# Performance work log

Measured on AMD Instinct MI355X. Metric: run time of the kernel, lower is better.

## Reference

```python
import jax, jax.numpy as jnp
import numpy as np

B, N, D, P = 4, 512, 512, 128

def setup_inputs() -> dict:
    key = jax.random.key(0)
    ks = jax.random.split(key, 8)
    s = lambda fan_in: 1.0 / np.sqrt(fan_in)
    inp = {
        "input": jax.random.normal(ks[0], (B, N, D), dtype=jnp.float32),
        # bigram projections (weights stored [in, out]; torch Linear is [out, in])
        "Wl": jax.random.uniform(ks[1], (D, P), jnp.float32, -s(D), s(D)),
        "bl": jnp.zeros((P,), jnp.float32),  # zeroed in initialize_parameters
        "Wr": jax.random.uniform(ks[2], (D, P), jnp.float32, -s(D), s(D)),  # no bias
        "Wo": jax.random.uniform(ks[3], (P, 1), jnp.float32, -s(P), s(P)),
        "bo": jnp.zeros((1,), jnp.float32),
        # start builder MLP
        "Ws1": jax.random.uniform(ks[4], (D, P), jnp.float32, -s(D), s(D)),
        "bs1": jnp.zeros((P,), jnp.float32),
        "Ws2": jax.random.uniform(ks[5], (P, 1), jnp.float32, -s(P), s(P)),
        "bs2": jnp.zeros((1,), jnp.float32),
        # end builder MLP
        "We1": jax.random.uniform(ks[6], (D, P), jnp.float32, -s(D), s(D)),
        "be1": jnp.zeros((P,), jnp.float32),
        "We2": jax.random.uniform(ks[7], (P, 1), jnp.float32, -s(P), s(P)),
        "be2": jnp.zeros((1,), jnp.float32),
    }
    return inp


def reference(input, Wl, bl, Wr, Wo, bo, Ws1, bs1, Ws2, bs2, We1, be1, We2, be2):
    # start / end unigram scores: [B, N, 1]
    start = jnp.maximum(input @ Ws1 + bs1, 0.0) @ Ws2 + bs2
    end = jnp.maximum(input @ We1 + be1, 0.0) @ We2 + be2
    # bigram scores
    left = input @ Wl + bl   # [B, N, P]
    right = input @ Wr       # [B, N, P]
    # left.unsqueeze(1) + right.unsqueeze(2) -> [B, N, N, P]
    proj = left[:, None, :, :] + right[:, :, None, :]
    bigram = jnp.maximum(proj, 0.0) @ Wo + bo  # [B, N, N, 1]
    return (bigram, start, end)
```

## Files before the change

kernel.cpp:

```cpp
#include <hip/hip_runtime.h>

typedef unsigned short ushort_t;
using f32x4  = __attribute__((ext_vector_type(4))) float;
using bf16x8 = __attribute__((ext_vector_type(8))) short;
using u16x8  = __attribute__((ext_vector_type(8))) unsigned short;

constexpr int Bc = 4;
constexpr int Nc = 512;
constexpr int Dc = 512;
constexpr int Pc = 128;
constexpr int ROWS = Bc * Nc;

__device__ inline unsigned short f2bf(float f) {
    unsigned u = __builtin_bit_cast(unsigned, f);
    unsigned r = u + 0x7fffu + ((u >> 16) & 1u);
    return (unsigned short)(r >> 16);
}

__device__ inline void gload_lds16(const void* g, void* l) {
    __builtin_amdgcn_global_load_lds(
        (const __attribute__((address_space(1))) unsigned int*)g,
        (__attribute__((address_space(3))) unsigned int*)l, 16, 0, 0);
}

__global__ __launch_bounds__(256) void convert_kernel(
    const float* __restrict__ input,
    const float* __restrict__ Wl,  const float* __restrict__ Wr,
    const float* __restrict__ Ws1, const float* __restrict__ We1,
    ushort_t* __restrict__ inBF2, ushort_t* __restrict__ WcatT2)
{
    const int bx = blockIdx.x, t = threadIdx.x;
    __shared__ float T[64][68];

    if (bx < 256) {
        const int mt = bx >> 3, ks = bx & 7;
        const int c = t & 7, r0 = t >> 3;
        const float* src = input + (size_t)(mt * 64) * Dc + ks * 64;
        ushort_t* dstc = inBF2 + ((size_t)(mt * 8 + ks) * 8 + c) * 512;
        #pragma unroll
        for (int h = 0; h < 2; ++h) {
            const int r = r0 + h * 32;
            const float* s = src + (size_t)r * Dc + c * 8;
            float4 v0 = *(const float4*)s;
            float4 v1 = *(const float4*)(s + 4);
            u16x8 o;
            o[0] = f2bf(v0.x); o[1] = f2bf(v0.y); o[2] = f2bf(v0.z); o[3] = f2bf(v0.w);
            o[4] = f2bf(v1.x); o[5] = f2bf(v1.y); o[6] = f2bf(v1.z); o[7] = f2bf(v1.w);
            *(u16x8*)(dstc + r * 8) = o;
        }
    } else {
        const int idx = bx - 256;
        const int nt = idx >> 3, ks = idx & 7;
        const int mi = nt >> 1, cm0 = (nt & 1) * 64;
        const float* Wm = (mi == 0) ? Wl : (mi == 1) ? Wr : (mi == 2) ? Ws1 : We1;

        const int kk_ = t >> 4, cc = (t & 15) << 2;
        #pragma unroll
        for (int u = 0; u < 4; ++u)
            *(float4*)&T[kk_ + 16 * u][cc] =
                *(const float4*)&Wm[(size_t)(ks * 64 + kk_ + 16 * u) * Pc + cm0 + cc];
        __syncthreads();

        const int col = t & 63, c2 = t >> 6;
        #pragma unroll
        for (int h = 0; h < 2; ++h) {
            const int kc = c2 + h * 4;
            u16x8 o;
            #pragma unroll
            for (int i = 0; i < 8; ++i) o[i] = f2bf(T[kc * 8 + i][col]);
            *(u16x8*)(WcatT2 + ((size_t)(nt * 8 + ks) * 8 + kc) * 512 + col * 8) = o;
        }
    }
}

__global__ __launch_bounds__(256) void mfma_proj2(
    const ushort_t* __restrict__ inBF2, const ushort_t* __restrict__ WcatT2,
    const float* __restrict__ bl,
    const float* __restrict__ bs1, const float* __restrict__ Ws2,
    const float* __restrict__ be1, const float* __restrict__ We2,
    float* __restrict__ left, float* __restrict__ right,
    float* __restrict__ parts)
{
    const int mt = blockIdx.x, ny = blockIdx.y;
    const int row0 = mt * 64;
    const int t = threadIdx.x, w = t >> 6, l = t & 63;
    const int wm = w >> 1, wn = w & 1;
    const int fr = l & 15, fg = l >> 4;

    __shared__ ushort_t As2[2][4096];
    __shared__ ushort_t Bs2[2][4096];
    __shared__ float red[2][64];

    const ushort_t* Abase = inBF2  + (size_t)mt * 8 * 4096;
    const ushort_t* Bbase = WcatT2 + (size_t)ny * 8 * 4096;

    f32x4 acc[2][2];
    #pragma unroll
    for (int m = 0; m < 2; ++m)
        #pragma unroll
        for (int n = 0; n < 2; ++n)
            acc[m][n] = f32x4{0.f, 0.f, 0.f, 0.f};

    const int c0 = 2 * w, c1 = 2 * w + 1;

#define STAGE(BI, KS)                                                        \
    {                                                                        \
        const ushort_t* ga = Abase + (KS) * 4096;                            \
        const ushort_t* gb = Bbase + (KS) * 4096;                            \
        gload_lds16(ga + c0 * 512 + l * 8, &As2[BI][c0 * 512]);              \
        gload_lds16(ga + c1 * 512 + l * 8, &As2[BI][c1 * 512]);              \
        gload_lds16(gb + c0 * 512 + l * 8, &Bs2[BI][c0 * 512]);              \
        gload_lds16(gb + c1 * 512 + l * 8, &Bs2[BI][c1 * 512]);              \
    }

    STAGE(0, 0);
    __syncthreads();

    for (int ks = 0; ks < 8; ++ks) {
        const int bi = ks & 1;
        if (ks < 7) STAGE(bi ^ 1, ks + 1);
        #pragma unroll
        for (int kk = 0; kk < 2; ++kk) {
            const int kc = kk * 4 + fg;
            bf16x8 a0 = *(const bf16x8*)&As2[bi][(kc * 64 + wm * 32 + fr) * 8];
            bf16x8 a1 = *(const bf16x8*)&As2[bi][(kc * 64 + wm * 32 + 16 + fr) * 8];
            bf16x8 b0 = *(const bf16x8*)&Bs2[bi][(kc * 64 + wn * 32 + fr) * 8];
            bf16x8 b1 = *(const bf16x8*)&Bs2[bi][(kc * 64 + wn * 32 + 16 + fr) * 8];
            acc[0][0] = __builtin_amdgcn_mfma_f32_16x16x32_bf16(a0, b0, acc[0][0], 0, 0, 0);
            acc[0][1] = __builtin_amdgcn_mfma_f32_16x16x32_bf16(a0, b1, acc[0][1], 0, 0, 0);
            acc[1][0] = __builtin_amdgcn_mfma_f32_16x16x32_bf16(a1, b0, acc[1][0], 0, 0, 0);
            acc[1][1] = __builtin_amdgcn_mfma_f32_16x16x32_bf16(a1, b1, acc[1][1], 0, 0, 0);
        }
        __syncthreads();
    }
#undef STAGE

    const int fq4 = fg << 2;
    if (ny < 4) {
        float* outp = (ny < 2) ? left : right;
        const int cbase = (ny & 1) * 64 + wn * 32;
        #pragma unroll
        for (int m = 0; m < 2; ++m) {
            const int row = row0 + wm * 32 + m * 16 + fq4;
            #pragma unroll
            for (int n = 0; n < 2; ++n) {
                const int col = cbase + n * 16 + fr;
                const float bv = (ny < 2) ? bl[col] : 0.f;
                #pragma unroll
                for (int q = 0; q < 4; ++q)
                    outp[(size_t)(row + q) * Pc + col] = acc[m][n][q] + bv;
            }
        }
    } else {
        const float* b1 = (ny < 6) ? bs1 : be1;
        const float* W2 = (ny < 6) ? Ws2 : We2;
        const int pbase = (ny < 6) ? (ny - 4) * 64 : (ny - 6) * 64;
        float vs[2][4];
        #pragma unroll
        for (int m = 0; m < 2; ++m)
            #pragma unroll
            for (int q = 0; q < 4; ++q) {
                float v = 0.f;
                #pragma unroll
                for (int n = 0; n < 2; ++n) {
                    const int cp = pbase + wn * 32 + n * 16 + fr;
                    v += fmaxf(acc[m][n][q] + b1[cp], 0.f) * W2[cp];
                }
                v += __shfl_xor(v, 1);
                v += __shfl_xor(v, 2);
                v += __shfl_xor(v, 4);
                v += __shfl_xor(v, 8);
                vs[m][q] = v;
            }
        if (fr == 0) {
            #pragma unroll
            for (int m = 0; m < 2; ++m)
                #pragma unroll
                for (int q = 0; q < 4; ++q)
                    red[wn][wm * 32 + m * 16 + fq4 + q] = vs[m][q];
        }
        __syncthreads();
        if (t < 64) {
            const int pi = ny - 4;
            parts[pi * ROWS + row0 + t] = red[0][t] + red[1][t];
        }
    }
}

__global__ __launch_bounds__(256) void bigram_kernel(
    const float* __restrict__ left, const float* __restrict__ right,
    const float* __restrict__ Wo,   const float* __restrict__ bo,
    const float* __restrict__ parts,
    const float* __restrict__ bs2,  const float* __restrict__ be2,
    float* __restrict__ out, float* __restrict__ start_out,
    float* __restrict__ end_out)
{
    const int jt = blockIdx.x, it = blockIdx.y, b = blockIdx.z;
    const int t  = threadIdx.x;

    if (jt == 8) {
        if (it >= 8) return;
        const int base = (b * 8 + it) * 64;
        if (t < 64) {
            const int r = base + t;
            start_out[r] = parts[r] + parts[ROWS + r] + bs2[0];
        } else if (t < 128) {
            const int r = base + t - 64;
            end_out[r] = parts[2 * ROWS + r] + parts[3 * ROWS + r] + be2[0];
        }
        return;
    }

    __shared__ float Ls[64][132];
    __shared__ float Rs[32][132];
    __shared__ float wos[Pc];

    const float* lp = left  + (size_t)(b * Nc + jt * 64) * Pc;
    const float* rp = right + (size_t)(b * Nc + it * 32) * Pc;

    #pragma unroll
    for (int u = 0; u < 8; ++u) {
        int f = t + u * 256, r = f >> 5, p4 = (f & 31) << 2;
        *(float4*)&Ls[r][p4] = *(const float4*)&lp[r * Pc + p4];
    }
    #pragma unroll
    for (int u = 0; u < 4; ++u) {
        int f = t + u * 256, r = f >> 5, p4 = (f & 31) << 2;
        *(float4*)&Rs[r][p4] = *(const float4*)&rp[r * Pc + p4];
    }
    if (t < 32) *(float4*)&wos[t << 2] = *(const float4*)&Wo[t << 2];
    __syncthreads();

    const int jl = t & 15;
    const int il = t >> 4;

    float acc[2][4] = {};

#define LOADG(P, W4, L4, R4)                                             \
    {                                                                    \
        W4 = *(const float4*)&wos[(P)];                                  \
        _Pragma("unroll") for (int jj = 0; jj < 4; ++jj)                 \
            L4[jj] = *(const float4*)&Ls[jl + 16 * jj][(P)];             \
        _Pragma("unroll") for (int ii = 0; ii < 2; ++ii)                 \
            R4[ii] = *(const float4*)&Rs[il + 16 * ii][(P)];             \
    }

#define COMPUTE(W4, L4, R4)                                              \
    {                                                                    \
        _Pragma("unroll") for (int ii = 0; ii < 2; ++ii)                 \
        _Pragma("unroll") for (int jj = 0; jj < 4; ++jj) {               \
            acc[ii][jj] = fmaf(fmaxf(L4[jj].x + R4[ii].x, 0.f), W4.x, acc[ii][jj]); \
            acc[ii][jj] = fmaf(fmaxf(L4[jj].y + R4[ii].y, 0.f), W4.y, acc[ii][jj]); \
            acc[ii][jj] = fmaf(fmaxf(L4[jj].z + R4[ii].z, 0.f), W4.z, acc[ii][jj]); \
            acc[ii][jj] = fmaf(fmaxf(L4[jj].w + R4[ii].w, 0.f), W4.w, acc[ii][jj]); \
        }                                                                \
    }

    float4 wa, la[4], ra[2];
    float4 wb, lb4[4], rb4[2];
    LOADG(0, wa, la, ra);

    #pragma unroll 1
    for (int p = 0; p < Pc; p += 8) {
        LOADG(p + 4, wb, lb4, rb4);
        COMPUTE(wa, la, ra);
        if (p + 8 < Pc) LOADG(p + 8, wa, la, ra);
        COMPUTE(wb, lb4, rb4);
    }

    const float bias = bo[0];
    #pragma unroll
    for (int ii = 0; ii < 2; ++ii) {
        #pragma unroll
        for (int jj = 0; jj < 4; ++jj) {
            const int gi = it * 32 + il + 16 * ii;
            const int gj = jt * 64 + jl + 16 * jj;
            out[((size_t)b * Nc + gi) * Nc + gj] = acc[ii][jj] + bias;
        }
    }
#undef LOADG
#undef COMPUTE
}

extern "C" void kernel_launch(void* const* d_in, const int* in_sizes, int n_in,
                              void* d_out, int out_size, void* d_ws, size_t ws_size,
                              hipStream_t stream) {
    const float* input = (const float*)d_in[0];
    const float* Wl  = (const float*)d_in[1];
    const float* bl  = (const float*)d_in[2];
    const float* Wr  = (const float*)d_in[3];
    const float* Wo  = (const float*)d_in[4];
    const float* bo  = (const float*)d_in[5];
    const float* Ws1 = (const float*)d_in[6];
    const float* bs1 = (const float*)d_in[7];
    const float* Ws2 = (const float*)d_in[8];
    const float* bs2 = (const float*)d_in[9];
    const float* We1 = (const float*)d_in[10];
    const float* be1 = (const float*)d_in[11];
    const float* We2 = (const float*)d_in[12];
    const float* be2 = (const float*)d_in[13];

    float* out    = (float*)d_out;
    float* bigram = out;
    float* start  = out + (size_t)Bc * Nc * Nc;
    float* end    = start + (size_t)Bc * Nc;

    float* left   = (float*)d_ws;
    float* right  = left + (size_t)ROWS * Pc;
    float* parts  = right + (size_t)ROWS * Pc;
    ushort_t* inBF2  = (ushort_t*)(parts + 4 * ROWS);
    ushort_t* WcatT2 = inBF2 + (size_t)ROWS * Dc;

    convert_kernel<<<320, 256, 0, stream>>>(input, Wl, Wr, Ws1, We1, inBF2, WcatT2);

    mfma_proj2<<<dim3(32, 8), 256, 0, stream>>>(
        inBF2, WcatT2, bl, bs1, Ws2, be1, We2, left, right, parts);

    bigram_kernel<<<dim3(9, 16, 4), 256, 0, stream>>>(
        left, right, Wo, bo, parts, bs2, be2, bigram, start, end);
}
```

Before: 38.18 us.

## Store left/right projections in fp16 and use packed half dot2 in bigram

The projection kernel now writes left/right as fp16 instead of fp32. The bigram kernel does the add and ReLU as packed half2 operations and accumulates through v_dot2_f32_f16 into fp32. The bigram tile is reshaped to 32 columns by 64 rows, and the grid changes to match. This halves workspace traffic and roughly halves VALU instruction count in the dominant N×N×P loop, at the cost of fp16 rounding in the intermediate sums.

```diff
diff --git a/kernel.cpp b/kernel.cpp
--- a/kernel.cpp
+++ b/kernel.cpp
@@ -4,6 +4,7 @@
 using f32x4  = __attribute__((ext_vector_type(4))) float;
 using bf16x8 = __attribute__((ext_vector_type(8))) short;
 using u16x8  = __attribute__((ext_vector_type(8))) unsigned short;
+using h2v    = __attribute__((ext_vector_type(2))) _Float16;
 
 constexpr int Bc = 4;
 constexpr int Nc = 512;
@@ -21,6 +22,12 @@
     __builtin_amdgcn_global_load_lds(
         (const __attribute__((address_space(1))) unsigned int*)g,
         (__attribute__((address_space(3))) unsigned int*)l, 16, 0, 0);
+}
+
+__device__ inline unsigned packh2(float a, float b) {
+    unsigned short lo = __builtin_bit_cast(unsigned short, (_Float16)a);
+    unsigned short hi = __builtin_bit_cast(unsigned short, (_Float16)b);
+    return (unsigned)lo | ((unsigned)hi << 16);
 }
 
 __global__ __launch_bounds__(256) void convert_kernel(
@@ -78,7 +85,7 @@
     const float* __restrict__ bl,
     const float* __restrict__ bs1, const float* __restrict__ Ws2,
     const float* __restrict__ be1, const float* __restrict__ We2,
-    float* __restrict__ left, float* __restrict__ right,
+    ushort_t* __restrict__ leftH, ushort_t* __restrict__ rightH,
     float* __restrict__ parts)
 {
     const int mt = blockIdx.x, ny = blockIdx.y;
@@ -137,7 +144,7 @@
 
     const int fq4 = fg << 2;
     if (ny < 4) {
-        float* outp = (ny < 2) ? left : right;
+        ushort_t* outp = (ny < 2) ? leftH : rightH;
         const int cbase = (ny & 1) * 64 + wn * 32;
         #pragma unroll
         for (int m = 0; m < 2; ++m) {
@@ -147,8 +154,11 @@
                 const int col = cbase + n * 16 + fr;
                 const float bv = (ny < 2) ? bl[col] : 0.f;
                 #pragma unroll
-                for (int q = 0; q < 4; ++q)
-                    outp[(size_t)(row + q) * Pc + col] = acc[m][n][q] + bv;
+                for (int q = 0; q < 4; ++q) {
+                    float v = acc[m][n][q] + bv;
+                    outp[(size_t)(row + q) * Pc + col] =
+                        __builtin_bit_cast(ushort_t, (_Float16)v);
+                }
             }
         }
     } else {
@@ -188,7 +198,7 @@
 }
 
 __global__ __launch_bounds__(256) void bigram_kernel(
-    const float* __restrict__ left, const float* __restrict__ right,
+    const ushort_t* __restrict__ leftH, const ushort_t* __restrict__ rightH,
     const float* __restrict__ Wo,   const float* __restrict__ bo,
     const float* __restrict__ parts,
     const float* __restrict__ bs2,  const float* __restrict__ be2,
@@ -198,8 +208,7 @@
     const int jt = blockIdx.x, it = blockIdx.y, b = blockIdx.z;
     const int t  = threadIdx.x;
 
-    if (jt == 8) {
-        if (it >= 8) return;
+    if (jt == 16) {
         const int base = (b * 8 + it) * 64;
         if (t < 64) {
             const int r = base + t;
@@ -211,75 +220,75 @@
         return;
     }
 
-    __shared__ float Ls[64][132];
-    __shared__ float Rs[32][132];
-    __shared__ float wos[Pc];
-
-    const float* lp = left  + (size_t)(b * Nc + jt * 64) * Pc;
-    const float* rp = right + (size_t)(b * Nc + it * 32) * Pc;
+    __shared__ unsigned Lh[32][68];
+    __shared__ unsigned Rh[64][68];
+    __shared__ unsigned woh[64];
+
+    const ushort_t* lp = leftH  + (size_t)(b * Nc + jt * 32) * Pc;
+    const ushort_t* rp = rightH + (size_t)(b * Nc + it * 64) * Pc;
 
     #pragma unroll
-    for (int u = 0; u < 8; ++u) {
-        int f = t + u * 256, r = f >> 5, p4 = (f & 31) << 2;
-        *(float4*)&Ls[r][p4] = *(const float4*)&lp[r * Pc + p4];
+    for (int u = 0; u < 2; ++u) {
+        int f = t + u * 256, r = f >> 4, c = f & 15;
+        *(float4*)&Lh[r][c * 4] = *(const float4*)(lp + (size_t)r * Pc + c * 8);
     }
     #pragma unroll
     for (int u = 0; u < 4; ++u) {
-        int f = t + u * 256, r = f >> 5, p4 = (f & 31) << 2;
-        *(float4*)&Rs[r][p4] = *(const float4*)&rp[r * Pc + p4];
-    }
-    if (t < 32) *(float4*)&wos[t << 2] = *(const float4*)&Wo[t << 2];
+        int f = t + u * 256, r = f >> 4, c = f & 15;
+        *(float4*)&Rh[r][c * 4] = *(const float4*)(rp + (size_t)r * Pc + c * 8);
+    }
+    if (t < 64) woh[t] = packh2(Wo[2 * t], Wo[2 * t + 1]);
     __syncthreads();
 
     const int jl = t & 15;
     const int il = t >> 4;
 
-    float acc[2][4] = {};
-
-#define LOADG(P, W4, L4, R4)                                             \
-    {                                                                    \
-        W4 = *(const float4*)&wos[(P)];                                  \
-        _Pragma("unroll") for (int jj = 0; jj < 4; ++jj)                 \
-            L4[jj] = *(const float4*)&Ls[jl + 16 * jj][(P)];             \
-        _Pragma("unroll") for (int ii = 0; ii < 2; ++ii)                 \
-            R4[ii] = *(const float4*)&Rs[il + 16 * ii][(P)];             \
-    }
-
-#define COMPUTE(W4, L4, R4)                                              \
-    {                                                                    \
-        _Pragma("unroll") for (int ii = 0; ii < 2; ++ii)                 \
-        _Pragma("unroll") for (int jj = 0; jj < 4; ++jj) {               \
-            acc[ii][jj] = fmaf(fmaxf(L4[jj].x + R4[ii].x, 0.f), W4.x, acc[ii][jj]); \
-            acc[ii][jj] = fmaf(fmaxf(L4[jj].y + R4[ii].y, 0.f), W4.y, acc[ii][jj]); \
-            acc[ii][jj] = fmaf(fmaxf(L4[jj].z + R4[ii].z, 0.f), W4.z, acc[ii][jj]); \
-            acc[ii][jj] = fmaf(fmaxf(L4[jj].w + R4[ii].w, 0.f), W4.w, acc[ii][jj]); \
-        }                                                                \
-    }
-
-    float4 wa, la[4], ra[2];
-    float4 wb, lb4[4], rb4[2];
-    LOADG(0, wa, la, ra);
-
-    #pragma unroll 1
-    for (int p = 0; p < Pc; p += 8) {
-        LOADG(p + 4, wb, lb4, rb4);
-        COMPUTE(wa, la, ra);
-        if (p + 8 < Pc) LOADG(p + 8, wa, la, ra);
-        COMPUTE(wb, lb4, rb4);
+    float acc[4][2] = {};
+    const h2v hz = {(_Float16)0.f, (_Float16)0.f};
+
+    #pragma unroll 8
+    for (int s = 0; s < 32; ++s) {
+        uint2 w2 = *(const uint2*)&woh[2 * s];
+        uint2 l2[2], r2[4];
+        #pragma unroll
+        for (int jj = 0; jj < 2; ++jj) l2[jj] = *(const uint2*)&Lh[jl + 16 * jj][2 * s];
+        #pragma unroll
+        for (int ii = 0; ii < 4; ++ii) r2[ii] = *(const uint2*)&Rh[il + 16 * ii][2 * s];
+
+        #pragma unroll
+        for (int h = 0; h < 2; ++h) {
+            const unsigned wu = h ? w2.y : w2.x;
+            h2v lv[2], rv[4];
+            #pragma unroll
+            for (int jj = 0; jj < 2; ++jj)
+                lv[jj] = __builtin_bit_cast(h2v, h ? l2[jj].y : l2[jj].x);
+            #pragma unroll
+            for (int ii = 0; ii < 4; ++ii)
+                rv[ii] = __builtin_bit_cast(h2v, h ? r2[ii].y : r2[ii].x);
+            #pragma unroll
+            for (int ii = 0; ii < 4; ++ii) {
+                #pragma unroll
+                for (int jj = 0; jj < 2; ++jj) {
+                    h2v sum = lv[jj] + rv[ii];
+                    sum = __builtin_elementwise_max(sum, hz);
+                    unsigned su = __builtin_bit_cast(unsigned, sum);
+                    asm("v_dot2_f32_f16 %0, %1, %2, %0"
+                        : "+v"(acc[ii][jj]) : "v"(su), "v"(wu));
+                }
+            }
+        }
     }
 
     const float bias = bo[0];
     #pragma unroll
-    for (int ii = 0; ii < 2; ++ii) {
-        #pragma unroll
-        for (int jj = 0; jj < 4; ++jj) {
-            const int gi = it * 32 + il + 16 * ii;
-            const int gj = jt * 64 + jl + 16 * jj;
+    for (int ii = 0; ii < 4; ++ii) {
+        #pragma unroll
+        for (int jj = 0; jj < 2; ++jj) {
+            const int gi = it * 64 + il + 16 * ii;
+            const int gj = jt * 32 + jl + 16 * jj;
             out[((size_t)b * Nc + gi) * Nc + gj] = acc[ii][jj] + bias;
         }
     }
-#undef LOADG
-#undef COMPUTE
 }
 
 extern "C" void kernel_launch(void* const* d_in, const int* in_sizes, int n_in,
@@ -305,17 +314,17 @@
     float* start  = out + (size_t)Bc * Nc * Nc;
     float* end    = start + (size_t)Bc * Nc;
 
-    float* left   = (float*)d_ws;
-    float* right  = left + (size_t)ROWS * Pc;
-    float* parts  = right + (size_t)ROWS * Pc;
+    ushort_t* leftH  = (ushort_t*)d_ws;
+    ushort_t* rightH = leftH + (size_t)ROWS * Pc;
+    float* parts     = (float*)(rightH + (size_t)ROWS * Pc);
     ushort_t* inBF2  = (ushort_t*)(parts + 4 * ROWS);
     ushort_t* WcatT2 = inBF2 + (size_t)ROWS * Dc;
 
     convert_kernel<<<320, 256, 0, stream>>>(input, Wl, Wr, Ws1, We1, inBF2, WcatT2);
 
     mfma_proj2<<<dim3(32, 8), 256, 0, stream>>>(
-        inBF2, WcatT2, bl, bs1, Ws2, be1, We2, left, right, parts);
-
-    bigram_kernel<<<dim3(9, 16, 4), 256, 0, stream>>>(
-        left, right, Wo, bo, parts, bs2, be2, bigram, start, end);
-}
+        inBF2, WcatT2, bl, bs1, Ws2, be1, We2, leftH, rightH, parts);
+
+    bigram_kernel<<<dim3(17, 8, 4), 256, 0, stream>>>(
+        leftH, rightH, Wo, bo, parts, bs2, be2, bigram, start, end);
+}
```

Result: faster. 31.52 us (-17.4%).
